# Optimization experiments

Hardware: AMD Instinct MI355X
Metric: run time of the kernel (lower is better)

The kernel has to match this reference:

```python
import jax, jax.numpy as jnp
import numpy as np

N = 50000
E = 800000
NEG_SLOPE = 0.2  # PyG GATConv default


def gat_conv(x, src, dst, W, att_src, att_dst, bias, heads, out_ch, concat):
    # x: [N, F_in]; W: [F_in, heads*out_ch]; att_*: [heads, out_ch]; bias: [heads*out_ch] or [out_ch]
    h = (x @ W).reshape(N, heads, out_ch)                       # [N, H, C]
    a_src = jnp.sum(h * att_src, axis=-1)                       # [N, H]
    a_dst = jnp.sum(h * att_dst, axis=-1)                       # [N, H]
    e = jax.nn.leaky_relu(a_src[src] + a_dst[dst], NEG_SLOPE)   # [E', H]
    # numerically stable scatter-softmax over incoming edges of each dst node
    e_max = jax.ops.segment_max(e, dst, num_segments=N)         # [N, H]
    ex = jnp.exp(e - e_max[dst])                                # [E', H]
    denom = jax.ops.segment_sum(ex, dst, num_segments=N)        # [N, H]
    alpha = ex / denom[dst]                                     # [E', H]
    msg = h[src] * alpha[:, :, None]                            # [E', H, C]
    out = jax.ops.segment_sum(msg, dst, num_segments=N)         # [N, H, C]
    out = out.reshape(N, heads * out_ch) if concat else out.mean(axis=1)
    return out + bias


def setup_inputs() -> dict:
    key = jax.random.key(0)
    ks = jax.random.split(key, 16)
    s = 0.05
    x = jax.random.normal(ks[0], (N, 128), dtype=jnp.float32)
    edge_index = jax.random.randint(ks[1], (2, E), 0, N, dtype=jnp.int64)
    H, C = 8, 64
    return {
        "x": x,
        "edge_index": edge_index,
        "W0": jax.random.normal(ks[2], (128, H * C), dtype=jnp.float32) * s,
        "as0": jax.random.normal(ks[3], (H, C), dtype=jnp.float32) * s,
        "ad0": jax.random.normal(ks[4], (H, C), dtype=jnp.float32) * s,
        "b0": jnp.zeros((H * C,), dtype=jnp.float32),
        "W1": jax.random.normal(ks[5], (H * C, H * C), dtype=jnp.float32) * s,
        "as1": jax.random.normal(ks[6], (H, C), dtype=jnp.float32) * s,
        "ad1": jax.random.normal(ks[7], (H, C), dtype=jnp.float32) * s,
        "b1": jnp.zeros((H * C,), dtype=jnp.float32),
        "W2": jax.random.normal(ks[8], (H * C, 40), dtype=jnp.float32) * s,
        "as2": jax.random.normal(ks[9], (1, 40), dtype=jnp.float32) * s,
        "ad2": jax.random.normal(ks[10], (1, 40), dtype=jnp.float32) * s,
        "b2": jnp.zeros((40,), dtype=jnp.float32),
    }


def reference(x, edge_index, W0, as0, ad0, b0, W1, as1, ad1, b1, W2, as2, ad2, b2):
    # add self-loops (PyG GATConv default add_self_loops=True)
    loop = jnp.arange(N, dtype=edge_index.dtype)
    src = jnp.concatenate([edge_index[0], loop])
    dst = jnp.concatenate([edge_index[1], loop])
    h = gat_conv(x, src, dst, W0, as0, ad0, b0, heads=8, out_ch=64, concat=True)
    h = jax.nn.relu(h)  # dropout is identity at inference
    h = gat_conv(h, src, dst, W1, as1, ad1, b1, heads=8, out_ch=64, concat=True)
    h = jax.nn.relu(h)
    h = gat_conv(h, src, dst, W2, as2, ad2, b2, heads=1, out_ch=40, concat=False)
    return jax.nn.log_softmax(h, axis=1)
```

## Files before the change

### kernel.cpp

```cpp
#include <hip/hip_runtime.h>
#include <hip/hip_bf16.h>
#include <math.h>

#define N_NODES 50000
#define N_EDGES 800000
#define TOT_EDGES (N_EDGES + N_NODES)
#define NEG_SLOPE 0.2f
#define M_PAD 50048
#define N_CHUNKS ((N_NODES + 1023) / 1024)

typedef __attribute__((ext_vector_type(8))) short bf16x8;
typedef __attribute__((ext_vector_type(4))) float f32x4;

__device__ __forceinline__ unsigned short f2bf(float f){
  union { float f; unsigned u; } x; x.f = f;
  unsigned r = x.u + 0x7FFF + ((x.u >> 16) & 1);
  return (unsigned short)(r >> 16);
}
__device__ __forceinline__ float bf2f(unsigned short h){
  union { unsigned u; float f; } x; x.u = ((unsigned)h) << 16;
  return x.f;
}
__device__ __forceinline__ void gl_lds16(const void* g, void* l){
  __builtin_amdgcn_global_load_lds(
    (const __attribute__((address_space(1))) unsigned int*)g,
    (__attribute__((address_space(3))) unsigned int*)l, 16, 0, 0);
}


__global__ void hist_kernel(const int* __restrict__ ei, int* __restrict__ counts){
  int e = blockIdx.x*256 + threadIdx.x;
  if (e >= TOT_EDGES) return;
  int d = (e < N_EDGES) ? ei[N_EDGES + e] : (e - N_EDGES);
  atomicAdd(&counts[d], 1);
}

__global__ void scan1_kernel(const int* __restrict__ counts, int* __restrict__ partial,
                             int* __restrict__ chunksum){
  __shared__ int sm[1024];
  int t = threadIdx.x;
  int idx = blockIdx.x*1024 + t;
  int v = (idx < N_NODES) ? counts[idx] : 0;
  sm[t] = v;
  __syncthreads();
  for (int off = 1; off < 1024; off <<= 1){
    int u = (t >= off) ? sm[t-off] : 0;
    __syncthreads();
    sm[t] += u;
    __syncthreads();
  }
  if (idx < N_NODES) partial[idx] = sm[t];
  if (t == 1023) chunksum[blockIdx.x] = sm[1023];
}

__global__ void scan2_kernel(const int* __restrict__ chunksum, int* __restrict__ carry){
  if (threadIdx.x == 0){
    int c = 0;
    for (int i = 0; i < N_CHUNKS; ++i){ carry[i] = c; c += chunksum[i]; }
  }
}

__global__ void scan3_kernel(const int* __restrict__ partial, const int* __restrict__ counts,
                             const int* __restrict__ carry, int* __restrict__ offsets,
                             int* __restrict__ cursor){
  int idx = blockIdx.x*256 + threadIdx.x;
  if (idx >= N_NODES) return;
  int inc = partial[idx] + carry[idx >> 10];
  offsets[idx+1] = inc;
  cursor[idx] = inc - counts[idx];
  if (idx == 0) offsets[0] = 0;
}

__global__ void scatter_kernel(const int* __restrict__ ei, int* __restrict__ cursor,
                               int* __restrict__ ssrc){
  int e = blockIdx.x*256 + threadIdx.x;
  if (e >= TOT_EDGES) return;
  int s, d;
  if (e < N_EDGES){ s = ei[e]; d = ei[N_EDGES+e]; } else { s = e - N_EDGES; d = s; }
  int pos = atomicAdd(&cursor[d], 1);
  ssrc[pos] = s;
}


__global__ void convert_BT(const float* __restrict__ B, unsigned short* __restrict__ BTh,
                           unsigned short* __restrict__ BTl, int K, int N){
  int id = blockIdx.x*256 + threadIdx.x;
  if (id >= K*N) return;
  int n = id / K, k = id - n*K;
  float v = B[(size_t)k*N + n];
  unsigned short h = f2bf(v);
  unsigned short l = f2bf(v - bf2f(h));
  BTh[id] = h; BTl[id] = l;
}

__global__ void convert_BT2(const float* __restrict__ B, unsigned short* __restrict__ BTh,
                            unsigned short* __restrict__ BTl){
  int id = blockIdx.x*256 + threadIdx.x;
  if (id >= 128*512) return;
  int n = id >> 9, k = id & 511;
  float v = (n < 40) ? B[(size_t)k*40 + n] : 0.f;
  unsigned short h = f2bf(v);
  unsigned short l = f2bf(v - bf2f(h));
  BTh[id] = h; BTl[id] = l;
}


__global__ __launch_bounds__(256, 2) void mfma_gemm(
    const float* __restrict__ A, const unsigned short* __restrict__ BTh,
    const unsigned short* __restrict__ BTl, float* __restrict__ C,
    unsigned short* __restrict__ Fb,
    const float* __restrict__ att_s, const float* __restrict__ att_d,
    float* __restrict__ asrc, float* __restrict__ adst,
    int M, int K, int Nc)
{
  __shared__ unsigned short sAh[128*32];
  __shared__ unsigned short sAl[128*32];
  __shared__ unsigned short sBh[128*32];
  __shared__ unsigned short sBl[128*32];

  const int tid = threadIdx.x;
  const int lane = tid & 63;
  const int wid = tid >> 6;
  const int wr = wid >> 1, wc = wid & 1;
  const int bm = blockIdx.y * 128, bn = blockIdx.x * 128;
  const int lr = lane & 15, kg = lane >> 4;

  const float* aread[4];
  int awoff[4];
  #pragma unroll
  for (int i = 0; i < 4; ++i){
    int o = tid + i*256;
    int row = o >> 3, ch = o & 7;
    int gr = bm + row; if (gr > M-1) gr = M-1;
    aread[i] = A + (size_t)gr*K + ch*4;
    int sc = (ch >> 1) ^ ((row >> 1) & 3);
    awoff[i] = row*32 + sc*8 + (ch & 1)*4;
  }
  size_t bgoff[2];
  #pragma unroll
  for (int i = 0; i < 2; ++i){
    int o = tid + i*256;
    int row = o >> 2, ch = o & 3;
    int sc = ch ^ ((row >> 1) & 3);
    bgoff[i] = (size_t)(bn + row)*K + sc*8;
  }
  int aoff[4], boff[4];
  #pragma unroll
  for (int i = 0; i < 4; ++i){
    int row = wr*64 + i*16 + lr;
    aoff[i] = row*32 + (kg ^ ((row >> 1) & 3))*8;
    int col = wc*64 + i*16 + lr;
    boff[i] = col*32 + (kg ^ ((col >> 1) & 3))*8;
  }

  float4 areg[4];
  auto loadA = [&](int k0){
    #pragma unroll
    for (int i = 0; i < 4; ++i)
      areg[i] = *(const float4*)(aread[i] + k0);
  };
  auto writeA = [&](){
    #pragma unroll
    for (int i = 0; i < 4; ++i){
      float4 v = areg[i];
      ushort4 h, l;
      h.x = f2bf(v.x); l.x = f2bf(v.x - bf2f(h.x));
      h.y = f2bf(v.y); l.y = f2bf(v.y - bf2f(h.y));
      h.z = f2bf(v.z); l.z = f2bf(v.z - bf2f(h.z));
      h.w = f2bf(v.w); l.w = f2bf(v.w - bf2f(h.w));
      *(ushort4*)&sAh[awoff[i]] = h;
      *(ushort4*)&sAl[awoff[i]] = l;
    }
  };
  auto stageB = [&](int k0){
    #pragma unroll
    for (int i = 0; i < 2; ++i){
      gl_lds16(BTh + bgoff[i] + k0, &sBh[(tid + i*256)*8]);
      gl_lds16(BTl + bgoff[i] + k0, &sBl[(tid + i*256)*8]);
    }
  };

  f32x4 acc[4][4];
  #pragma unroll
  for (int i = 0; i < 4; ++i)
    #pragma unroll
    for (int j = 0; j < 4; ++j)
      acc[i][j] = (f32x4){0.f, 0.f, 0.f, 0.f};

  loadA(0); writeA(); stageB(0);
  __syncthreads();
  int k0 = 0;
  while (true){
    int kn = k0 + 32;
    if (kn < K) loadA(kn);
    bf16x8 ah[4], al[4], bh[4], bl[4];
    #pragma unroll
    for (int i = 0; i < 4; ++i){
      ah[i] = *(const bf16x8*)&sAh[aoff[i]];
      al[i] = *(const bf16x8*)&sAl[aoff[i]];
      bh[i] = *(const bf16x8*)&sBh[boff[i]];
      bl[i] = *(const bf16x8*)&sBl[boff[i]];
    }
    #pragma unroll
    for (int i = 0; i < 4; ++i)
      #pragma unroll
      for (int j = 0; j < 4; ++j){
        acc[i][j] = __builtin_amdgcn_mfma_f32_16x16x32_bf16(ah[i], bh[j], acc[i][j], 0, 0, 0);
        acc[i][j] = __builtin_amdgcn_mfma_f32_16x16x32_bf16(al[i], bh[j], acc[i][j], 0, 0, 0);
        acc[i][j] = __builtin_amdgcn_mfma_f32_16x16x32_bf16(ah[i], bl[j], acc[i][j], 0, 0, 0);
      }
    if (kn >= K) break;
    __syncthreads();
    writeA();
    stageB(kn);
    __syncthreads();
    k0 = kn;
  }

  if (att_s){
    int head = (bn >> 6) + wc;
    float ws_[4], wd_[4];
    #pragma unroll
    for (int j = 0; j < 4; ++j){
      ws_[j] = att_s[head*64 + j*16 + lr];
      wd_[j] = att_d[head*64 + j*16 + lr];
    }
    #pragma unroll
    for (int i = 0; i < 4; ++i){
      #pragma unroll
      for (int r = 0; r < 4; ++r){
        float vs = 0.f, vd = 0.f;
        #pragma unroll
        for (int j = 0; j < 4; ++j){
          vs += acc[i][j][r] * ws_[j];
          vd += acc[i][j][r] * wd_[j];
        }
        #pragma unroll
        for (int m = 1; m < 16; m <<= 1){
          vs += __shfl_xor(vs, m);
          vd += __shfl_xor(vd, m);
        }
        int gm = bm + wr*64 + i*16 + kg*4 + r;
        if ((lane & 15) == 0 && gm < M){
          asrc[gm*8 + head] = vs;
          adst[gm*8 + head] = vd;
        }
      }
    }
  }

  #pragma unroll
  for (int i = 0; i < 4; ++i){
    int gm0 = bm + wr*64 + i*16 + kg*4;
    #pragma unroll
    for (int j = 0; j < 4; ++j){
      int gn = bn + wc*64 + j*16 + lr;
      #pragma unroll
      for (int r = 0; r < 4; ++r){
        int gm = gm0 + r;
        if (gm < M){
          if (C && gn < Nc) C[(size_t)gm*Nc + gn] = acc[i][j][r];
          if (Fb) Fb[(size_t)gm*512 + gn] = f2bf(acc[i][j][r]);
        }
      }
    }
  }
}


__global__ __launch_bounds__(256) void aggregate_kernel(const unsigned short* __restrict__ Fb,
    const int* __restrict__ offsets, const int* __restrict__ ssrc,
    const float* __restrict__ asrc, const float* __restrict__ adst,
    const float* __restrict__ bias, float* __restrict__ OUT, int do_relu){
  int d = blockIdx.x;
  int t = threadIdx.x;
  int beg = offsets[d], end = offsets[d+1];
  int deg = end - beg;
  __shared__ float red[256];
  __shared__ float mh[8], invd[8];
  __shared__ float al[32][8];
  __shared__ int sArr[32];
  int hh = t & 7, grp = t >> 3;
  float ad = adst[d*8 + hh];
  float pm = -1e30f;
  for (int i = grp; i < deg; i += 32){
    int s = ssrc[beg+i];
    float e = asrc[s*8+hh] + ad;
    e = (e > 0.f) ? e : NEG_SLOPE*e;
    pm = fmaxf(pm, e);
  }
  red[t] = pm; __syncthreads();
  #pragma unroll
  for (int off = 128; off >= 8; off >>= 1){
    if (t < off) red[t] = fmaxf(red[t], red[t+off]);
    __syncthreads();
  }
  if (t < 8) mh[t] = red[t];
  __syncthreads();
  float m = mh[hh];
  float ps = 0.f;
  for (int i = grp; i < deg; i += 32){
    int s = ssrc[beg+i];
    float e = asrc[s*8+hh] + ad;
    e = (e > 0.f) ? e : NEG_SLOPE*e;
    ps += __expf(e - m);
  }
  red[t] = ps; __syncthreads();
  #pragma unroll
  for (int off = 128; off >= 8; off >>= 1){
    if (t < off) red[t] += red[t+off];
    __syncthreads();
  }
  if (t < 8) invd[t] = 1.f / red[t];
  __syncthreads();
  int c = t*2;
  int h = t >> 5;
  float acc0 = 0.f, acc1 = 0.f;
  for (int i0 = 0; i0 < deg; i0 += 32){
    int nch = min(32, deg - i0);
    float alv = 0.f;
    if (grp < nch){
      int s = ssrc[beg + i0 + grp];
      float e = asrc[s*8+hh] + ad;
      e = (e > 0.f) ? e : NEG_SLOPE*e;
      alv = __expf(e - mh[hh]) * invd[hh];
      if (hh == 0) sArr[grp] = s;
    }
    al[grp][hh] = alv;
    __syncthreads();
    #pragma unroll 2
    for (int i = 0; i < nch; ++i){
      unsigned v = *(const unsigned*)&Fb[(size_t)sArr[i]*512 + c];
      union { unsigned u; float f; } lo, hi;
      lo.u = v << 16;
      hi.u = v & 0xffff0000u;
      float a = al[i][h];
      acc0 += a * lo.f;
      acc1 += a * hi.f;
    }
    __syncthreads();
  }
  float2 bb = ((const float2*)bias)[t];
  float o0 = acc0 + bb.x, o1 = acc1 + bb.y;
  if (do_relu){ o0 = fmaxf(o0, 0.f); o1 = fmaxf(o1, 0.f); }
  ((float2*)(OUT + (size_t)d*512))[t] = make_float2(o0, o1);
}


__global__ void attn_coef2_kernel(const float* __restrict__ H2v, const float* __restrict__ as2,
                                  const float* __restrict__ ad2,
                                  float* __restrict__ asrc, float* __restrict__ adst){
  int gid = blockIdx.x*256 + threadIdx.x;
  int node = gid >> 6;
  int lane = threadIdx.x & 63;
  if (node >= N_NODES) return;
  float v = 0.f, ws = 0.f, wd = 0.f;
  if (lane < 40){ v = H2v[(size_t)node*40 + lane]; ws = as2[lane]; wd = ad2[lane]; }
  float vs = v*ws, vd = v*wd;
  #pragma unroll
  for (int off = 32; off > 0; off >>= 1){
    vs += __shfl_down(vs, off);
    vd += __shfl_down(vd, off);
  }
  if (lane == 0){ asrc[node] = vs; adst[node] = vd; }
}

__global__ __launch_bounds__(64) void aggregate2_kernel(const float* __restrict__ H2v,
    const int* __restrict__ offsets, const int* __restrict__ ssrc,
    const float* __restrict__ asrc, const float* __restrict__ adst,
    const float* __restrict__ bias, float* __restrict__ OUT){
  int d = blockIdx.x;
  int lane = threadIdx.x;
  int beg = offsets[d], end = offsets[d+1];
  int deg = end - beg;
  float ad = adst[d];
  float pm = -1e30f;
  for (int i = lane; i < deg; i += 64){
    int s = ssrc[beg+i];
    float e = asrc[s] + ad; e = (e>0.f)?e:NEG_SLOPE*e;
    pm = fmaxf(pm, e);
  }
  #pragma unroll
  for (int off = 32; off > 0; off >>= 1) pm = fmaxf(pm, __shfl_xor(pm, off));
  float ps = 0.f;
  for (int i = lane; i < deg; i += 64){
    int s = ssrc[beg+i];
    float e = asrc[s] + ad; e=(e>0.f)?e:NEG_SLOPE*e;
    ps += __expf(e - pm);
  }
  #pragma unroll
  for (int off = 32; off > 0; off >>= 1) ps += __shfl_xor(ps, off);
  float inv = 1.f/ps;
  __shared__ float alS[64];
  __shared__ int sS[64];
  float acc = 0.f;
  for (int i0 = 0; i0 < deg; i0 += 64){
    int nch = min(64, deg - i0);
    if (lane < nch){
      int s = ssrc[beg+i0+lane];
      float e = asrc[s]+ad; e=(e>0.f)?e:NEG_SLOPE*e;
      alS[lane] = __expf(e-pm)*inv;
      sS[lane] = s;
    }
    __syncthreads();
    for (int i = 0; i < nch; ++i){
      if (lane < 40) acc += alS[i] * H2v[(size_t)sS[i]*40 + lane];
    }
    __syncthreads();
  }
  float logit = (lane<40) ? (acc + bias[lane]) : -1e30f;
  float mm = logit;
  #pragma unroll
  for (int off = 32; off > 0; off >>= 1) mm = fmaxf(mm, __shfl_xor(mm, off));
  float ex = (lane<40) ? __expf(logit-mm) : 0.f;
  float ss = ex;
  #pragma unroll
  for (int off = 32; off > 0; off >>= 1) ss += __shfl_xor(ss, off);
  if (lane < 40) OUT[(size_t)d*40 + lane] = logit - mm - logf(ss);
}


extern "C" void kernel_launch(void* const* d_in, const int* in_sizes, int n_in,
                              void* d_out, int out_size, void* d_ws, size_t ws_size,
                              hipStream_t stream){
  const float* x   = (const float*)d_in[0];
  const int*   ei  = (const int*)d_in[1];
  const float* W0  = (const float*)d_in[2];
  const float* as0 = (const float*)d_in[3];
  const float* ad0 = (const float*)d_in[4];
  const float* b0  = (const float*)d_in[5];
  const float* W1  = (const float*)d_in[6];
  const float* as1 = (const float*)d_in[7];
  const float* ad1 = (const float*)d_in[8];
  const float* b1  = (const float*)d_in[9];
  const float* W2  = (const float*)d_in[10];
  const float* as2 = (const float*)d_in[11];
  const float* ad2 = (const float*)d_in[12];
  const float* b2  = (const float*)d_in[13];
  float* out = (float*)d_out;

  char* p = (char*)d_ws;
  auto alloc = [&](size_t bytes)->void*{
    void* r = (void*)p; p += (bytes + 255) & ~(size_t)255; return r;
  };
  float* F1    = (float*)alloc((size_t)M_PAD*512*4);
  unsigned short* Fb = (unsigned short*)alloc((size_t)M_PAD*512*2);
  float* ASRC  = (float*)alloc((size_t)N_NODES*8*4);
  float* ADST  = (float*)alloc((size_t)N_NODES*8*4);
  float* H2v   = (float*)alloc((size_t)N_NODES*40*4);
  float* ASRC2 = (float*)alloc((size_t)N_NODES*4);
  float* ADST2 = (float*)alloc((size_t)N_NODES*4);
  int* counts  = (int*)alloc((size_t)N_NODES*4);
  int* offsets = (int*)alloc((size_t)(N_NODES+1)*4);
  int* cursor  = (int*)alloc((size_t)N_NODES*4);
  int* ssrc    = (int*)alloc((size_t)TOT_EDGES*4);
  int* partial = (int*)alloc((size_t)N_NODES*4);
  int* chunksum= (int*)alloc(64*4);
  int* carry   = (int*)alloc(64*4);
  unsigned short* BTh  = (unsigned short*)alloc((size_t)512*512*2);
  unsigned short* BTl  = (unsigned short*)alloc((size_t)512*512*2);
  unsigned short* BT2h = (unsigned short*)alloc((size_t)128*512*2);
  unsigned short* BT2l = (unsigned short*)alloc((size_t)128*512*2);

  hipMemsetAsync(counts, 0, (size_t)N_NODES*4, stream);
  hist_kernel<<<(TOT_EDGES+255)/256, 256, 0, stream>>>(ei, counts);
  scan1_kernel<<<N_CHUNKS, 1024, 0, stream>>>(counts, partial, chunksum);
  scan2_kernel<<<1, 64, 0, stream>>>(chunksum, carry);
  scan3_kernel<<<(N_NODES+255)/256, 256, 0, stream>>>(partial, counts, carry, offsets, cursor);
  scatter_kernel<<<(TOT_EDGES+255)/256, 256, 0, stream>>>(ei, cursor, ssrc);

  int mt = M_PAD / 128;

  convert_BT<<<(128*512+255)/256, 256, 0, stream>>>(W0, BTh, BTl, 128, 512);
  mfma_gemm<<<dim3(4, mt), 256, 0, stream>>>(x, BTh, BTl, nullptr, Fb,
                                             as0, ad0, ASRC, ADST, N_NODES, 128, 512);
  aggregate_kernel<<<N_NODES, 256, 0, stream>>>(Fb, offsets, ssrc, ASRC, ADST, b0, F1, 1);

  convert_BT<<<(512*512+255)/256, 256, 0, stream>>>(W1, BTh, BTl, 512, 512);
  mfma_gemm<<<dim3(4, mt), 256, 0, stream>>>(F1, BTh, BTl, nullptr, Fb,
                                             as1, ad1, ASRC, ADST, N_NODES, 512, 512);
  aggregate_kernel<<<N_NODES, 256, 0, stream>>>(Fb, offsets, ssrc, ASRC, ADST, b1, F1, 1);

  convert_BT2<<<(128*512+255)/256, 256, 0, stream>>>(W2, BT2h, BT2l);
  mfma_gemm<<<dim3(1, mt), 256, 0, stream>>>(F1, BT2h, BT2l, H2v, nullptr,
                                             nullptr, nullptr, nullptr, nullptr, N_NODES, 512, 40);
  attn_coef2_kernel<<<(N_NODES*64+255)/256, 256, 0, stream>>>(H2v, as2, ad2, ASRC2, ADST2);
  aggregate2_kernel<<<N_NODES, 64, 0, stream>>>(H2v, offsets, ssrc, ASRC2, ADST2, b2, out);
}
```

Before: 740.4 us.

## Split GAT aggregation into softmax-stats kernel and column-sliced SpMM kernel

Replaces the one-block-per-node aggregate kernel with two kernels. The first computes the per-node, per-head softmax max and inverse denominator, one wave per node, using shuffle reductions instead of shared-memory reductions. The second is an SpMM with a 2D grid: 16 column slices of 32 channels and 8 nodes per block, recomputing each alpha inline with no barriers. This drops the many __syncthreads per node and improves occupancy, at the cost of 2-byte bf16 gathers instead of 4-byte ones and of recomputing exp for every channel lane.

```diff
diff --git a/kernel.cpp b/kernel.cpp
--- a/kernel.cpp
+++ b/kernel.cpp
@@ -268,82 +268,74 @@
 }
 
 
-__global__ __launch_bounds__(256) void aggregate_kernel(const unsigned short* __restrict__ Fb,
+__global__ __launch_bounds__(256) void softmax_stats(const int* __restrict__ offsets,
+    const int* __restrict__ ssrc, const float* __restrict__ asrc,
+    const float* __restrict__ adst, float* __restrict__ mx, float* __restrict__ inv){
+  int w = threadIdx.x >> 6;
+  int lane = threadIdx.x & 63;
+  int d = blockIdx.x*4 + w;
+  if (d >= N_NODES) return;
+  int h = lane & 7, grp = lane >> 3;
+  int beg = offsets[d], end = offsets[d+1];
+  float ad = adst[d*8+h];
+  float pm = -1e30f;
+  for (int i = beg+grp; i < end; i += 8){
+    int s = ssrc[i];
+    float e = asrc[s*8+h] + ad;
+    e = (e > 0.f) ? e : NEG_SLOPE*e;
+    pm = fmaxf(pm, e);
+  }
+  pm = fmaxf(pm, __shfl_xor(pm, 8));
+  pm = fmaxf(pm, __shfl_xor(pm, 16));
+  pm = fmaxf(pm, __shfl_xor(pm, 32));
+  float ps = 0.f;
+  for (int i = beg+grp; i < end; i += 8){
+    int s = ssrc[i];
+    float e = asrc[s*8+h] + ad;
+    e = (e > 0.f) ? e : NEG_SLOPE*e;
+    ps += __expf(e - pm);
+  }
+  ps += __shfl_xor(ps, 8);
+  ps += __shfl_xor(ps, 16);
+  ps += __shfl_xor(ps, 32);
+  if (grp == 0){ mx[d*8+h] = pm; inv[d*8+h] = 1.f/ps; }
+}
+
+
+__global__ __launch_bounds__(256) void spmm_kernel(const unsigned short* __restrict__ Fb,
     const int* __restrict__ offsets, const int* __restrict__ ssrc,
     const float* __restrict__ asrc, const float* __restrict__ adst,
+    const float* __restrict__ mx, const float* __restrict__ inv,
     const float* __restrict__ bias, float* __restrict__ OUT, int do_relu){
-  int d = blockIdx.x;
-  int t = threadIdx.x;
+  int slice = blockIdx.y;
+  int h = slice >> 1;
+  int c = slice*32 + (threadIdx.x & 31);
+  int g = threadIdx.x >> 5;
+  int d = blockIdx.x*8 + g;
+  if (d >= N_NODES) return;
   int beg = offsets[d], end = offsets[d+1];
-  int deg = end - beg;
-  __shared__ float red[256];
-  __shared__ float mh[8], invd[8];
-  __shared__ float al[32][8];
-  __shared__ int sArr[32];
-  int hh = t & 7, grp = t >> 3;
-  float ad = adst[d*8 + hh];
-  float pm = -1e30f;
-  for (int i = grp; i < deg; i += 32){
-    int s = ssrc[beg+i];
-    float e = asrc[s*8+hh] + ad;
-    e = (e > 0.f) ? e : NEG_SLOPE*e;
-    pm = fmaxf(pm, e);
-  }
-  red[t] = pm; __syncthreads();
-  #pragma unroll
-  for (int off = 128; off >= 8; off >>= 1){
-    if (t < off) red[t] = fmaxf(red[t], red[t+off]);
-    __syncthreads();
-  }
-  if (t < 8) mh[t] = red[t];
-  __syncthreads();
-  float m = mh[hh];
-  float ps = 0.f;
-  for (int i = grp; i < deg; i += 32){
-    int s = ssrc[beg+i];
-    float e = asrc[s*8+hh] + ad;
-    e = (e > 0.f) ? e : NEG_SLOPE*e;
-    ps += __expf(e - m);
-  }
-  red[t] = ps; __syncthreads();
-  #pragma unroll
-  for (int off = 128; off >= 8; off >>= 1){
-    if (t < off) red[t] += red[t+off];
-    __syncthreads();
-  }
-  if (t < 8) invd[t] = 1.f / red[t];
-  __syncthreads();
-  int c = t*2;
-  int h = t >> 5;
-  float acc0 = 0.f, acc1 = 0.f;
-  for (int i0 = 0; i0 < deg; i0 += 32){
-    int nch = min(32, deg - i0);
-    float alv = 0.f;
-    if (grp < nch){
-      int s = ssrc[beg + i0 + grp];
-      float e = asrc[s*8+hh] + ad;
-      e = (e > 0.f) ? e : NEG_SLOPE*e;
-      alv = __expf(e - mh[hh]) * invd[hh];
-      if (hh == 0) sArr[grp] = s;
-    }
-    al[grp][hh] = alv;
-    __syncthreads();
-    #pragma unroll 2
-    for (int i = 0; i < nch; ++i){
-      unsigned v = *(const unsigned*)&Fb[(size_t)sArr[i]*512 + c];
-      union { unsigned u; float f; } lo, hi;
-      lo.u = v << 16;
-      hi.u = v & 0xffff0000u;
-      float a = al[i][h];
-      acc0 += a * lo.f;
-      acc1 += a * hi.f;
-    }
-    __syncthreads();
-  }
-  float2 bb = ((const float2*)bias)[t];
-  float o0 = acc0 + bb.x, o1 = acc1 + bb.y;
-  if (do_relu){ o0 = fmaxf(o0, 0.f); o1 = fmaxf(o1, 0.f); }
-  ((float2*)(OUT + (size_t)d*512))[t] = make_float2(o0, o1);
+  float ad = adst[d*8+h];
+  float m  = mx[d*8+h];
+  float iv = inv[d*8+h];
+  float acc = 0.f;
+  int i = beg;
+  for (; i+2 <= end; i += 2){
+    int s0 = ssrc[i], s1 = ssrc[i+1];
+    float f0 = bf2f(Fb[(size_t)s0*512 + c]);
+    float f1 = bf2f(Fb[(size_t)s1*512 + c]);
+    float e0 = asrc[s0*8+h] + ad; e0 = (e0>0.f)?e0:NEG_SLOPE*e0;
+    float e1 = asrc[s1*8+h] + ad; e1 = (e1>0.f)?e1:NEG_SLOPE*e1;
+    acc += __expf(e0-m)*iv * f0;
+    acc += __expf(e1-m)*iv * f1;
+  }
+  for (; i < end; ++i){
+    int s = ssrc[i];
+    float e = asrc[s*8+h] + ad; e = (e>0.f)?e:NEG_SLOPE*e;
+    acc += __expf(e-m)*iv * bf2f(Fb[(size_t)s*512 + c]);
+  }
+  float o = acc + bias[c];
+  if (do_relu) o = fmaxf(o, 0.f);
+  OUT[(size_t)d*512 + c] = o;
 }
 
 
@@ -447,6 +439,8 @@
   unsigned short* Fb = (unsigned short*)alloc((size_t)M_PAD*512*2);
   float* ASRC  = (float*)alloc((size_t)N_NODES*8*4);
   float* ADST  = (float*)alloc((size_t)N_NODES*8*4);
+  float* MX    = (float*)alloc((size_t)N_NODES*8*4);
+  float* INV   = (float*)alloc((size_t)N_NODES*8*4);
   float* H2v   = (float*)alloc((size_t)N_NODES*40*4);
   float* ASRC2 = (float*)alloc((size_t)N_NODES*4);
   float* ADST2 = (float*)alloc((size_t)N_NODES*4);
@@ -470,16 +464,19 @@
   scatter_kernel<<<(TOT_EDGES+255)/256, 256, 0, stream>>>(ei, cursor, ssrc);
 
   int mt = M_PAD / 128;
+  dim3 spmm_grid((N_NODES + 7) / 8, 16);
 
   convert_BT<<<(128*512+255)/256, 256, 0, stream>>>(W0, BTh, BTl, 128, 512);
   mfma_gemm<<<dim3(4, mt), 256, 0, stream>>>(x, BTh, BTl, nullptr, Fb,
                                              as0, ad0, ASRC, ADST, N_NODES, 128, 512);
-  aggregate_kernel<<<N_NODES, 256, 0, stream>>>(Fb, offsets, ssrc, ASRC, ADST, b0, F1, 1);
+  softmax_stats<<<(N_NODES+3)/4, 256, 0, stream>>>(offsets, ssrc, ASRC, ADST, MX, INV);
+  spmm_kernel<<<spmm_grid, 256, 0, stream>>>(Fb, offsets, ssrc, ASRC, ADST, MX, INV, b0, F1, 1);
 
   convert_BT<<<(512*512+255)/256, 256, 0, stream>>>(W1, BTh, BTl, 512, 512);
   mfma_gemm<<<dim3(4, mt), 256, 0, stream>>>(F1, BTh, BTl, nullptr, Fb,
                                              as1, ad1, ASRC, ADST, N_NODES, 512, 512);
-  aggregate_kernel<<<N_NODES, 256, 0, stream>>>(Fb, offsets, ssrc, ASRC, ADST, b1, F1, 1);
+  softmax_stats<<<(N_NODES+3)/4, 256, 0, stream>>>(offsets, ssrc, ASRC, ADST, MX, INV);
+  spmm_kernel<<<spmm_grid, 256, 0, stream>>>(Fb, offsets, ssrc, ASRC, ADST, MX, INV, b1, F1, 1);
 
   convert_BT2<<<(128*512+255)/256, 256, 0, stream>>>(W2, BT2h, BT2l);
   mfma_gemm<<<dim3(1, mt), 256, 0, stream>>>(F1, BT2h, BT2l, H2v, nullptr,
```

New measurement: 1.312 ms. 77.2% more time.
